# Optimization experiments

Measured on AMD Instinct MI355X. Metric: run time of the kernel, lower is better.

## Reference

```python
import jax, jax.numpy as jnp
import numpy as np

B, S, E, H = 16, 2048, 128, 128  # batch, seq_len, n_embd, head_dim


def setup_inputs() -> dict:
    key = jax.random.key(0)
    ks = jax.random.split(key, 6)
    init_s = 1.0 / np.sqrt(E)  # ~ torch Linear default init scale
    return {
        "q": jax.random.normal(ks[0], (B, S, E), jnp.float32),
        "k": jax.random.normal(ks[1], (B, S, E), jnp.float32),
        "v": jax.random.normal(ks[2], (B, S, E), jnp.float32),
        "Wq": jax.random.normal(ks[3], (H, E), jnp.float32) * init_s,
        "bq": jnp.zeros((H,), jnp.float32),
        "Wk": jax.random.normal(ks[4], (H, E), jnp.float32) * init_s,
        "bk": jnp.zeros((H,), jnp.float32),
        "Wv": jax.random.normal(ks[5], (H, E), jnp.float32) * init_s,
        "bv": jnp.zeros((H,), jnp.float32),
        "mask": jnp.tril(jnp.ones((S, S), jnp.float32)),  # causal mask
    }


def reference(q, k, v, Wq, bq, Wk, bk, Wv, bv, mask):
    # Linear projections: y = x @ W.T + b (torch nn.Linear convention)
    qh = q @ Wq.T + bq  # [B,S,H]
    kh = k @ Wk.T + bk  # [B,S,H]
    vh = v @ Wv.T + bv  # [B,S,H]
    d_k = kh.shape[-1]
    wei = jnp.einsum("bqd,bkd->bqk", qh, kh) * (d_k ** -0.5)  # [B,S,S]
    wei = jnp.where(mask == 0, -jnp.inf, wei)  # masked_fill(mask==0, -inf)
    attn = jax.nn.softmax(wei, axis=-1)
    return jnp.einsum("bqk,bkd->bqd", attn, vh)  # [B,S,H]
```

## Files before the change

### kernel.cpp

```cpp
#include <hip/hip_runtime.h>
#include <hip/hip_bf16.h>

#define BATCH 16
#define SEQ   2048
#define HD    128
#define TB    64
#define QB3   64
#define NT3   (SEQ/QB3)
#define PLANE ((size_t)BATCH*SEQ*HD)

typedef __attribute__((ext_vector_type(8))) short bf16x8;
typedef __attribute__((ext_vector_type(4))) float f32x4;
typedef __attribute__((ext_vector_type(2))) unsigned int u32x2;

#define MFMA(a,b,c) __builtin_amdgcn_mfma_f32_16x16x32_bf16(a,b,c,0,0,0)

__device__ __forceinline__ short f2bf(float f){
  union{float f; unsigned u;} v; v.f = f;
  unsigned r = (v.u + 0x7FFFu + ((v.u>>16)&1u))>>16;
  return (short)r;
}
__device__ __forceinline__ unsigned packbf(float lo, float hi){
  return ((unsigned)(unsigned short)f2bf(hi) << 16) | (unsigned short)f2bf(lo);
}
__device__ __forceinline__ bf16x8 pack8(f32x4 a, f32x4 b){
  bf16x8 r;
  r[0]=f2bf(a[0]); r[1]=f2bf(a[1]); r[2]=f2bf(a[2]); r[3]=f2bf(a[3]);
  r[4]=f2bf(b[0]); r[5]=f2bf(b[1]); r[6]=f2bf(b[2]); r[7]=f2bf(b[3]);
  return r;
}
__device__ __forceinline__ bf16x8 ldfrag(const float* base, size_t eo){
  const float* p = base + eo;
  return pack8(*(const f32x4*)p, *(const f32x4*)(p+4));
}

__global__ __launch_bounds__(256)
void wconv_kernel(const float* __restrict__ Wq, const float* __restrict__ Wk,
                  const float* __restrict__ Wv, short* __restrict__ wb)
{
  int i = (blockIdx.x*256 + threadIdx.x)*8;
  const float* src = (i < 16384) ? Wq : (i < 32768 ? Wk : Wv);
  int off = i & 16383;
  f32x4 a = *(const f32x4*)(src + off);
  f32x4 b = *(const f32x4*)(src + off + 4);
  *(bf16x8*)(wb + i) = pack8(a, b);
}

__global__ __launch_bounds__(256)
void proj_kernel(const float* __restrict__ k, const float* __restrict__ v,
                 const float* __restrict__ bk, const float* __restrict__ bv,
                 const short* __restrict__ wb, short* __restrict__ ws)
{
  __shared__ __align__(16) short T[TB*136];
  __shared__ __align__(16) short VT[HD*72];

  const int z = blockIdx.y + 1;
  const float* x  = (z==1) ? k  : v;
  const float* bb = (z==1) ? bk : bv;
  const short* W  = wb + (size_t)z*HD*HD;

  const int tid = threadIdx.x;
  const int w = tid>>6, l = tid&63, li = l&15, g = l>>4;
  const int bx = blockIdx.x;
  const int rowbase = bx*TB + w*16;

  bf16x8 afr[4];
  const float* xr = x + (size_t)(rowbase+li)*HD + g*8;
  #pragma unroll
  for (int ks=0; ks<4; ks++) afr[ks] = ldfrag(xr, (size_t)ks*32);

  f32x4 acc[8];
  #pragma unroll
  for (int ct=0; ct<8; ct++) acc[ct] = (f32x4){0.f,0.f,0.f,0.f};
  #pragma unroll
  for (int ct=0; ct<8; ct++){
    #pragma unroll
    for (int ks=0; ks<4; ks++){
      bf16x8 bfr = *(const bf16x8*)(W + (size_t)(ct*16+li)*HD + ks*32 + g*8);
      acc[ct] = MFMA(afr[ks], bfr, acc[ct]);
    }
  }

  const int img  = (bx>>1);
  const int half = bx & 1;

  if (z == 1){
    #pragma unroll
    for (int ct=0; ct<8; ct++){
      float bias = bb[ct*16+li];
      #pragma unroll
      for (int r=0; r<4; r++)
        T[(w*16+g*4+r)*136 + ct*16+li] = f2bf(acc[ct][r] + bias);
    }
    __syncthreads();
    short* dst = ws + PLANE + (size_t)img*16384;
    #pragma unroll
    for (int it=0; it<4; it++){
      int c = tid + it*256, row = c>>4, c8 = c&15;
      int r128 = half*64 + row;
      int chunk = r128*16 + (c8 ^ (r128&7));
      *(bf16x8*)(dst + chunk*8) = *(const bf16x8*)&T[row*136 + c8*8];
    }
  } else {
    #pragma unroll
    for (int ct=0; ct<8; ct++){
      float bias = bb[ct*16+li];
      #pragma unroll
      for (int r=0; r<4; r++)
        VT[(ct*16+li)*72 + w*16+g*4+r] = f2bf(acc[ct][r] + bias);
    }
    __syncthreads();
    short* dst = ws + 2*PLANE + (size_t)img*16384;
    const int d = tid>>1, hf = tid&1;
    #pragma unroll
    for (int j=0; j<4; j++){
      int c8l = hf*4 + j;
      int c8g = half*8 + c8l;
      int chunk = d*16 + (c8g ^ (d&7));
      *(bf16x8*)(dst + chunk*8) = *(const bf16x8*)&VT[d*72 + c8l*8];
    }
  }
}

__global__ __launch_bounds__(256, 2)
void attn_kernel(const float* __restrict__ qin, const float* __restrict__ bq,
                 const short* __restrict__ wb, const short* __restrict__ ws,
                 float* __restrict__ out)
{
  __shared__ __align__(16) short KVL[2][16384];
  __shared__ __align__(16) short PL[4][16*72];

  const int bid  = blockIdx.x;
  const int xcd  = bid & 7, slot = bid >> 3;
  const int b    = xcd*2 + (slot >> 5);
  const int sl   = slot & 31;
  const int qt   = (slot < 32) ? sl : (31 - sl);

  const int tid = threadIdx.x;
  const int w = tid>>6, l = tid&63, li = l&15, g = l>>4;

  const short* KimgB = ws + PLANE   + (size_t)b*(SEQ/128)*16384;
  const short* VimgB = ws + 2*PLANE + (size_t)b*(SEQ/128)*16384;

  const size_t qbase = (size_t)b*SEQ + qt*QB3;
  short* Pw = &PL[w][0];
  const float sc = 0.088388347648318447f;

  bf16x8 stg[8];
  #define LOADT(kt_) do{                                                     \
    const short* sK = KimgB + (size_t)((kt_)>>1)*16384 + ((kt_)&1)*8192;     \
    const short* sV = VimgB + (size_t)((kt_)>>1)*16384;                      \
    const int vh = ((kt_)&1)*8;                                              \
    _Pragma("unroll")                                                        \
    for (int j=0;j<4;j++) stg[j] = *(const bf16x8*)(sK + (tid + j*256)*8);   \
    _Pragma("unroll")                                                        \
    for (int j=0;j<4;j++){                                                   \
      int i = tid + j*256, d = i>>3, c8s = i&7;                              \
      stg[4+j] = *(const bf16x8*)(sV + (d*16 + vh + c8s)*8);                 \
    }                                                                        \
  }while(0)
  #define WRT(nb_) do{                                                      \
    short* dK = &KVL[nb_][0];                                               \
    short* dV = &KVL[nb_][8192];                                            \
    _Pragma("unroll")                                                       \
    for (int j=0;j<4;j++) *(bf16x8*)(dK + (tid+j*256)*8) = stg[j];          \
    _Pragma("unroll")                                                       \
    for (int j=0;j<4;j++) *(bf16x8*)(dV + (tid+j*256)*8) = stg[4+j];        \
  }while(0)

  LOADT(0);

  bf16x8 qfr[4];
  {
    bf16x8 xa[4];
    const float* xr = qin + (qbase + w*16 + li)*HD + g*8;
    #pragma unroll
    for (int ks=0; ks<4; ks++) xa[ks] = ldfrag(xr, (size_t)ks*32);
    f32x4 qa[8];
    #pragma unroll
    for (int ct=0; ct<8; ct++) qa[ct] = (f32x4){0.f,0.f,0.f,0.f};
    #pragma unroll
    for (int ct=0; ct<8; ct++){
      #pragma unroll
      for (int ks=0; ks<4; ks++){
        bf16x8 wf = *(const bf16x8*)(wb + (size_t)(ct*16+li)*HD + ks*32 + g*8);
        qa[ct] = MFMA(xa[ks], wf, qa[ct]);
      }
    }
    short* T = &KVL[0][0];
    #pragma unroll
    for (int ct=0; ct<8; ct++){
      float bias = bq[ct*16+li];
      #pragma unroll
      for (int r=0; r<4; r++)
        T[(w*16+g*4+r)*136 + ct*16+li] = f2bf(qa[ct][r] + bias);
    }
    __syncthreads();
    #pragma unroll
    for (int ks=0; ks<4; ks++)
      qfr[ks] = *(const bf16x8*)&T[(w*16+li)*136 + ks*32 + g*8];
    __syncthreads();
  }

  f32x4 oacc[8];
  #pragma unroll
  for (int dt=0; dt<8; dt++) oacc[dt] = (f32x4){0.f,0.f,0.f,0.f};
  float mreg = -1e30f, lreg = 0.f;

  WRT(0); __syncthreads();
  int cur = 0;

  for (int kt=0; kt<=qt; kt++){
    const bool pre = (kt < qt);
    if (pre) LOADT(kt+1);

    const short* KL = &KVL[cur][0];
    const short* VL = &KVL[cur][8192];

    f32x4 st[4];
    #pragma unroll
    for (int ct=0; ct<4; ct++) st[ct] = (f32x4){0.f,0.f,0.f,0.f};
    __builtin_amdgcn_s_setprio(1);
    #pragma unroll
    for (int ct=0; ct<4; ct++){
      const int row = ct*16 + li;
      #pragma unroll
      for (int ks=0; ks<4; ks++){
        const int chunk = row*16 + ((ks*4 + g) ^ (row&7));
        bf16x8 kfr = *(const bf16x8*)&KL[chunk*8];
        st[ct] = MFMA(kfr, qfr[ks], st[ct]);
      }
    }
    __builtin_amdgcn_s_setprio(0);

    float sv[4][4];
    float pm = -1e30f;
    const bool diag = (kt == qt);
    const int qloc = w*16 + li;
    #pragma unroll
    for (int ct=0; ct<4; ct++){
      #pragma unroll
      for (int r=0; r<4; r++){
        float x = st[ct][r]*sc;
        if (diag && (ct*16 + g*4 + r) > qloc) x = -1e30f;
        sv[ct][r] = x;
        pm = fmaxf(pm, x);
      }
    }
    pm = fmaxf(pm, __shfl_xor(pm, 16));
    pm = fmaxf(pm, __shfl_xor(pm, 32));
    float mn   = fmaxf(mreg, pm);
    float sclq = __expf(mreg - mn);
    mreg = mn;
    float psum = 0.f;
    #pragma unroll
    for (int ct=0; ct<4; ct++){
      #pragma unroll
      for (int r=0; r<4; r++){
        float p = __expf(sv[ct][r] - mn);
        sv[ct][r] = p;
        psum += p;
      }
    }
    psum += __shfl_xor(psum, 16);
    psum += __shfl_xor(psum, 32);
    lreg = lreg*sclq + psum;

    float sclo[4];
    #pragma unroll
    for (int r=0; r<4; r++) sclo[r] = __shfl(sclq, g*4 + r);
    #pragma unroll
    for (int dt=0; dt<8; dt++){
      #pragma unroll
      for (int r=0; r<4; r++) oacc[dt][r] *= sclo[r];
    }

    #pragma unroll
    for (int c4=0; c4<4; c4++){
      u32x2 pw;
      pw[0] = packbf(sv[c4][0], sv[c4][1]);
      pw[1] = packbf(sv[c4][2], sv[c4][3]);
      *(u32x2*)&Pw[li*72 + c4*16 + g*4] = pw;
    }
    __builtin_amdgcn_s_setprio(1);
    #pragma unroll
    for (int ks2=0; ks2<2; ks2++){
      bf16x8 afr = *(const bf16x8*)&Pw[li*72 + ks2*32 + g*8];
      #pragma unroll
      for (int dt=0; dt<8; dt++){
        const int d = dt*16 + li;
        const int chunk = d*8 + ((ks2*4 + g) ^ (d&7));
        bf16x8 bfr = *(const bf16x8*)&VL[chunk*8];
        oacc[dt] = MFMA(afr, bfr, oacc[dt]);
      }
    }
    __builtin_amdgcn_s_setprio(0);

    if (pre) WRT(cur^1);
    __syncthreads();
    cur ^= 1;
  }

  float lso[4];
  #pragma unroll
  for (int r=0; r<4; r++) lso[r] = __shfl(lreg, g*4 + r);
  float* Ob = out + qbase*HD;
  #pragma unroll
  for (int dt=0; dt<8; dt++){
    #pragma unroll
    for (int r=0; r<4; r++){
      Ob[(size_t)(w*16 + g*4 + r)*HD + dt*16 + li] = oacc[dt][r] / lso[r];
    }
  }
  #undef LOADT
  #undef WRT
}

extern "C" void kernel_launch(void* const* d_in, const int* in_sizes, int n_in,
                              void* d_out, int out_size, void* d_ws, size_t ws_size,
                              hipStream_t stream)
{
  short* ws = (short*)d_ws;
  short* wb = ws + 3*PLANE;

  wconv_kernel<<<24, 256, 0, stream>>>(
      (const float*)d_in[3], (const float*)d_in[5], (const float*)d_in[7], wb);

  dim3 pg(BATCH*SEQ/TB, 2);
  proj_kernel<<<pg, 256, 0, stream>>>(
      (const float*)d_in[1], (const float*)d_in[2],
      (const float*)d_in[6], (const float*)d_in[8],
      wb, ws);

  attn_kernel<<<dim3(BATCH*NT3), 256, 0, stream>>>(
      (const float*)d_in[0], (const float*)d_in[4], wb, ws, (float*)d_out);
}
```

Baseline: 96.24 us.

## Load K/V tiles directly into LDS and skip softmax rescale unless max grows

Result: slower. 99.92 us (+3.8%).

```diff
diff --git a/kernel.cpp b/kernel.cpp
--- a/kernel.cpp
+++ b/kernel.cpp
@@ -32,6 +32,11 @@
 __device__ __forceinline__ bf16x8 ldfrag(const float* base, size_t eo){
   const float* p = base + eo;
   return pack8(*(const f32x4*)p, *(const f32x4*)(p+4));
+}
+__device__ __forceinline__ void gload16(const short* g, short* l){
+  __builtin_amdgcn_global_load_lds(
+      (const __attribute__((address_space(1))) unsigned int*)g,
+      (__attribute__((address_space(3))) unsigned int*)l, 16, 0, 0);
 }
 
 __global__ __launch_bounds__(256)
@@ -146,29 +151,23 @@
   short* Pw = &PL[w][0];
   const float sc = 0.088388347648318447f;
 
-  bf16x8 stg[8];
-  #define LOADT(kt_) do{                                                     \
+  #define GLDS(kt_, nb_) do{                                                 \
     const short* sK = KimgB + (size_t)((kt_)>>1)*16384 + ((kt_)&1)*8192;     \
     const short* sV = VimgB + (size_t)((kt_)>>1)*16384;                      \
     const int vh = ((kt_)&1)*8;                                              \
+    short* dK = &KVL[nb_][0];                                                \
+    short* dV = &KVL[nb_][8192];                                             \
     _Pragma("unroll")                                                        \
-    for (int j=0;j<4;j++) stg[j] = *(const bf16x8*)(sK + (tid + j*256)*8);   \
+    for (int j=0;j<4;j++)                                                    \
+      gload16(sK + (tid + j*256)*8, dK + (w*64 + j*256)*8);                  \
     _Pragma("unroll")                                                        \
     for (int j=0;j<4;j++){                                                   \
       int i = tid + j*256, d = i>>3, c8s = i&7;                              \
-      stg[4+j] = *(const bf16x8*)(sV + (d*16 + vh + c8s)*8);                 \
+      gload16(sV + (d*16 + vh + c8s)*8, dV + (w*64 + j*256)*8);              \
     }                                                                        \
   }while(0)
-  #define WRT(nb_) do{                                                      \
-    short* dK = &KVL[nb_][0];                                               \
-    short* dV = &KVL[nb_][8192];                                            \
-    _Pragma("unroll")                                                       \
-    for (int j=0;j<4;j++) *(bf16x8*)(dK + (tid+j*256)*8) = stg[j];          \
-    _Pragma("unroll")                                                       \
-    for (int j=0;j<4;j++) *(bf16x8*)(dV + (tid+j*256)*8) = stg[4+j];        \
-  }while(0)
-
-  LOADT(0);
+
+  GLDS(0, 0);
 
   bf16x8 qfr[4];
   {
@@ -187,7 +186,7 @@
         qa[ct] = MFMA(xa[ks], wf, qa[ct]);
       }
     }
-    short* T = &KVL[0][0];
+    short* T = &KVL[1][0];
     #pragma unroll
     for (int ct=0; ct<8; ct++){
       float bias = bq[ct*16+li];
@@ -207,12 +206,11 @@
   for (int dt=0; dt<8; dt++) oacc[dt] = (f32x4){0.f,0.f,0.f,0.f};
   float mreg = -1e30f, lreg = 0.f;
 
-  WRT(0); __syncthreads();
   int cur = 0;
 
   for (int kt=0; kt<=qt; kt++){
     const bool pre = (kt < qt);
-    if (pre) LOADT(kt+1);
+    if (pre) GLDS(kt+1, cur^1);
 
     const short* KL = &KVL[cur][0];
     const short* VL = &KVL[cur][8192];
@@ -249,31 +247,33 @@
     }
     pm = fmaxf(pm, __shfl_xor(pm, 16));
     pm = fmaxf(pm, __shfl_xor(pm, 32));
-    float mn   = fmaxf(mreg, pm);
-    float sclq = __expf(mreg - mn);
-    mreg = mn;
+    if (!__all(pm - mreg <= 8.f)){
+      float mn   = fmaxf(mreg, pm);
+      float sclq = __expf(mreg - mn);
+      mreg = mn;
+      lreg *= sclq;
+      float sclo[4];
+      #pragma unroll
+      for (int r=0; r<4; r++) sclo[r] = __shfl(sclq, g*4 + r);
+      #pragma unroll
+      for (int dt=0; dt<8; dt++){
+        #pragma unroll
+        for (int r=0; r<4; r++) oacc[dt][r] *= sclo[r];
+      }
+    }
     float psum = 0.f;
     #pragma unroll
     for (int ct=0; ct<4; ct++){
       #pragma unroll
       for (int r=0; r<4; r++){
-        float p = __expf(sv[ct][r] - mn);
+        float p = __expf(sv[ct][r] - mreg);
         sv[ct][r] = p;
         psum += p;
       }
     }
     psum += __shfl_xor(psum, 16);
     psum += __shfl_xor(psum, 32);
-    lreg = lreg*sclq + psum;
-
-    float sclo[4];
-    #pragma unroll
-    for (int r=0; r<4; r++) sclo[r] = __shfl(sclq, g*4 + r);
-    #pragma unroll
-    for (int dt=0; dt<8; dt++){
-      #pragma unroll
-      for (int r=0; r<4; r++) oacc[dt][r] *= sclo[r];
-    }
+    lreg += psum;
 
     #pragma unroll
     for (int c4=0; c4<4; c4++){
@@ -296,7 +296,6 @@
     }
     __builtin_amdgcn_s_setprio(0);
 
-    if (pre) WRT(cur^1);
     __syncthreads();
     cur ^= 1;
   }
@@ -312,8 +311,7 @@
       Ob[(size_t)(w*16 + g*4 + r)*HD + dt*16 + li] = oacc[dt][r] / lso[r];
     }
   }
-  #undef LOADT
-  #undef WRT
+  #undef GLDS
 }
 
 extern "C" void kernel_launch(void* const* d_in, const int* in_sizes, int n_in,
```
